# Kernel optimization log

Measured on AMD Instinct MI355X. Metric: run time of the kernel, lower is better.

Reference implementation:

```python
import jax, jax.numpy as jnp
import numpy as np

HID = 512
B, M, N = 32, 2048, 2 * HID  # batch, src_len, 2*hid_size


def setup_inputs() -> dict:
    key = jax.random.key(0)
    ks = jax.random.split(key, 8)
    h_c_hat = jax.random.normal(ks[0], (B, N), dtype=jnp.float32)
    enc_outputs = jax.random.normal(ks[1], (B, M, N), dtype=jnp.float32)
    enc_feature = jax.random.normal(ks[2], (B * M, N), dtype=jnp.float32)
    enc_padding_mask = jnp.zeros((B, M), dtype=jnp.float32)  # 1.0 at PAD positions
    coverage = jax.random.uniform(ks[3], (B, M), dtype=jnp.float32)
    # learned params
    s = 1.0 / np.sqrt(N)
    Wd = jax.random.uniform(ks[4], (N, N), minval=-s, maxval=s, dtype=jnp.float32)  # decode_proj weight
    bd = jax.random.uniform(ks[5], (N,), minval=-s, maxval=s, dtype=jnp.float32)    # decode_proj bias
    wc = jax.random.uniform(ks[6], (N,), minval=-1.0, maxval=1.0, dtype=jnp.float32)  # w_c: Linear(1, 2h) weight
    v = jax.random.uniform(ks[7], (N,), minval=-s, maxval=s, dtype=jnp.float32)       # v: Linear(2h, 1) weight
    return {"h_c_hat": h_c_hat, "enc_outputs": enc_outputs, "enc_feature": enc_feature,
            "enc_padding_mask": enc_padding_mask, "coverage": coverage,
            "Wd": Wd, "bd": bd, "wc": wc, "v": v}


def reference(h_c_hat, enc_outputs, enc_feature, enc_padding_mask, coverage, Wd, bd, wc, v):
    b, m, n = enc_outputs.shape
    dec_feature = h_c_hat @ Wd.T + bd                      # [b, n]
    # enc_feature [b*m, n] + broadcast decoder feature + coverage feature (Linear(1,n) == outer product)
    att = enc_feature.reshape(b, m, n) + dec_feature[:, None, :] + coverage[:, :, None] * wc
    scores = jnp.tanh(att) @ v                             # [b, m]
    attn = jax.nn.softmax(scores, axis=1) * (1.0 - enc_padding_mask)
    attn = attn / attn.sum(axis=1, keepdims=True)          # renormalize after masking
    context_vec = jnp.einsum('bm,bmn->bn', attn, enc_outputs)  # [b, 2h]
    new_coverage = coverage + attn
    return context_vec, attn, new_coverage
```

## Files before the change

### kernel.cpp

```cpp
#include <hip/hip_runtime.h>
#include <math.h>

#define BB 32
#define MM 2048
#define NN 1024
#define C_SCALE 2.88539008177793f
#define L2E 1.44269504088896f

#if __has_builtin(__builtin_amdgcn_exp2f)
#define EXP2F(x) __builtin_amdgcn_exp2f(x)
#else
#define EXP2F(x) exp2f(x)
#endif
#if __has_builtin(__builtin_amdgcn_rcpf)
#define RCPF(x) __builtin_amdgcn_rcpf(x)
#else
#define RCPF(x) (1.0f / (x))
#endif

__device__ __forceinline__ float waveReduceSum(float x) {
#pragma unroll
    for (int off = 32; off > 0; off >>= 1) x += __shfl_xor(x, off, 64);
    return x;
}
__device__ __forceinline__ float waveReduceMax(float x) {
#pragma unroll
    for (int off = 32; off > 0; off >>= 1) x = fmaxf(x, __shfl_xor(x, off, 64));
    return x;
}

__global__ __launch_bounds__(256) void k_dec(const float* __restrict__ h,
                                             const float* __restrict__ Wd,
                                             const float* __restrict__ bd,
                                             float* __restrict__ dec_s) {
    const int n = blockIdx.x;
    const int t = threadIdx.x;
    const int lane = t & 63, wave = t >> 6;
    const float4 wd4 = *(const float4*)(Wd + (size_t)n * NN + t * 4);
    __shared__ float red[BB][4];
#pragma unroll
    for (int b = 0; b < BB; ++b) {
        const float4 h4 = *(const float4*)(h + b * NN + t * 4);
        float p = wd4.x * h4.x + wd4.y * h4.y + wd4.z * h4.z + wd4.w * h4.w;
        p = waveReduceSum(p);
        if (lane == 0) red[b][wave] = p;
    }
    __syncthreads();
    if (t < BB) {
        float s = red[t][0] + red[t][1] + red[t][2] + red[t][3];
        dec_s[t * NN + n] = (s + bd[n]) * C_SCALE;
    }
}

__global__ __launch_bounds__(256) void k_scores(const float* __restrict__ ef,
                                                const float* __restrict__ dec_s,
                                                const float* __restrict__ wc,
                                                const float* __restrict__ v,
                                                const float* __restrict__ cov,
                                                float* __restrict__ scores) {
    const int t = threadIdx.x;
    const int lane = t & 63, wave = t >> 6;
    const int b = blockIdx.x >> 5;
    const int mblk = blockIdx.x & 31;
    const int m0 = mblk * 64 + wave * 16;

    float4 dec4[4], wcs4[4], v4[4];
#pragma unroll
    for (int it = 0; it < 4; ++it) {
        const int k = it * 256 + lane * 4;
        dec4[it] = *(const float4*)(dec_s + b * NN + k);
        float4 w = *(const float4*)(wc + k);
        wcs4[it] = make_float4(w.x * C_SCALE, w.y * C_SCALE, w.z * C_SCALE, w.w * C_SCALE);
        v4[it] = *(const float4*)(v + k);
    }

    for (int mm = 0; mm < 16; ++mm) {
        const int m = m0 + mm;
        const float cv = cov[b * MM + m];
        const float* row = ef + (size_t)(b * MM + m) * NN;
        float acc = 0.f;
#pragma unroll
        for (int it = 0; it < 4; ++it) {
            const float4 e4 = *(const float4*)(row + it * 256 + lane * 4);
            {
                float x = fmaf(C_SCALE, e4.x, dec4[it].x); x = fmaf(cv, wcs4[it].x, x);
                float r = RCPF(EXP2F(x) + 1.0f);
                acc = fmaf(fmaf(-2.0f, r, 1.0f), v4[it].x, acc);
            }
            {
                float x = fmaf(C_SCALE, e4.y, dec4[it].y); x = fmaf(cv, wcs4[it].y, x);
                float r = RCPF(EXP2F(x) + 1.0f);
                acc = fmaf(fmaf(-2.0f, r, 1.0f), v4[it].y, acc);
            }
            {
                float x = fmaf(C_SCALE, e4.z, dec4[it].z); x = fmaf(cv, wcs4[it].z, x);
                float r = RCPF(EXP2F(x) + 1.0f);
                acc = fmaf(fmaf(-2.0f, r, 1.0f), v4[it].z, acc);
            }
            {
                float x = fmaf(C_SCALE, e4.w, dec4[it].w); x = fmaf(cv, wcs4[it].w, x);
                float r = RCPF(EXP2F(x) + 1.0f);
                acc = fmaf(fmaf(-2.0f, r, 1.0f), v4[it].w, acc);
            }
        }
        acc = waveReduceSum(acc);
        if (lane == 0) scores[b * MM + m] = acc;
    }
}

__global__ __launch_bounds__(256) void k_softmax(const float* __restrict__ scores,
                                                 const float* __restrict__ mask,
                                                 const float* __restrict__ cov,
                                                 float* __restrict__ attn_out,
                                                 float* __restrict__ cov_out) {
    const int b = blockIdx.x;
    const int t = threadIdx.x;
    const int lane = t & 63, wave = t >> 6;
    __shared__ float red[4];

    float s[8];
    float mx = -3.0e38f;
#pragma unroll
    for (int i = 0; i < 8; ++i) {
        s[i] = scores[b * MM + i * 256 + t];
        mx = fmaxf(mx, s[i]);
    }
    mx = waveReduceMax(mx);
    if (lane == 0) red[wave] = mx;
    __syncthreads();
    mx = fmaxf(fmaxf(red[0], red[1]), fmaxf(red[2], red[3]));
    __syncthreads();

    float g[8];
    float ls = 0.f;
#pragma unroll
    for (int i = 0; i < 8; ++i) {
        float keep = 1.0f - mask[b * MM + i * 256 + t];
        g[i] = EXP2F((s[i] - mx) * L2E) * keep;
        ls += g[i];
    }
    ls = waveReduceSum(ls);
    if (lane == 0) red[wave] = ls;
    __syncthreads();
    const float S = red[0] + red[1] + red[2] + red[3];
    const float inv = RCPF(S);
#pragma unroll
    for (int i = 0; i < 8; ++i) {
        const int idx = b * MM + i * 256 + t;
        const float a = g[i] * inv;
        attn_out[idx] = a;
        cov_out[idx] = cov[idx] + a;
    }
}

__global__ __launch_bounds__(256) void k_ctx_partial(const float* __restrict__ eo,
                                                     const float* __restrict__ attn,
                                                     float* __restrict__ part) {
    const int b = blockIdx.x >> 6;
    const int p = blockIdx.x & 63;
    const int t = threadIdx.x;
    const int n = t * 4;
    const float* base = eo + ((size_t)b * MM + p * 32) * NN + n;
    float4 acc = make_float4(0.f, 0.f, 0.f, 0.f);
#pragma unroll 4
    for (int mm = 0; mm < 32; ++mm) {
        const float a = attn[b * MM + p * 32 + mm];
        const float4 e = *(const float4*)(base + (size_t)mm * NN);
        acc.x = fmaf(a, e.x, acc.x);
        acc.y = fmaf(a, e.y, acc.y);
        acc.z = fmaf(a, e.z, acc.z);
        acc.w = fmaf(a, e.w, acc.w);
    }
    *(float4*)(part + ((size_t)(b * 64 + p)) * NN + n) = acc;
}

__global__ __launch_bounds__(256) void k_ctx_reduce(const float* __restrict__ part,
                                                    float* __restrict__ ctx) {
    const int idx = blockIdx.x * 256 + threadIdx.x;
    const int b = idx >> 10;
    const int n = idx & 1023;
    float s = 0.f;
#pragma unroll 8
    for (int p = 0; p < 64; ++p) s += part[((size_t)(b * 64 + p)) * NN + n];
    ctx[idx] = s;
}

extern "C" void kernel_launch(void* const* d_in, const int* in_sizes, int n_in,
                              void* d_out, int out_size, void* d_ws, size_t ws_size,
                              hipStream_t stream) {
    const float* h    = (const float*)d_in[0];
    const float* eo   = (const float*)d_in[1];
    const float* ef   = (const float*)d_in[2];
    const float* mask = (const float*)d_in[3];
    const float* cov  = (const float*)d_in[4];
    const float* Wd   = (const float*)d_in[5];
    const float* bd   = (const float*)d_in[6];
    const float* wc   = (const float*)d_in[7];
    const float* v    = (const float*)d_in[8];

    float* out  = (float*)d_out;
    float* ctx  = out;
    float* attn = out + BB * NN;
    float* ncov = attn + BB * MM;

    float* dec_s  = (float*)d_ws;
    float* scores = dec_s + BB * NN;
    float* part   = scores + BB * MM;

    k_dec<<<NN, 256, 0, stream>>>(h, Wd, bd, dec_s);
    k_scores<<<BB * 32, 256, 0, stream>>>(ef, dec_s, wc, v, cov, scores);
    k_softmax<<<BB, 256, 0, stream>>>(scores, mask, cov, attn, ncov);
    k_ctx_partial<<<BB * 64, 256, 0, stream>>>(eo, attn, part);
    k_ctx_reduce<<<(BB * NN) / 256, 256, 0, stream>>>(part, ctx);
}
```

Before: 544.9 us.

## Fuse softmax into score and context kernels using partial exp sums

Removes the standalone softmax kernel. The scores kernel now computes unnormalized exp(score)*keep directly, without subtracting the row max, and writes per-block partial sums. The context kernel reduces those partial sums to a normalizer, scales the weights on the fly, and writes attn and the new coverage. The scores grid is also split into twice as many blocks, each covering half as many rows. This saves a launch and a pass over the scores, but without the max subtraction exp can overflow if scores get large.

```diff
diff --git a/kernel.cpp b/kernel.cpp
--- a/kernel.cpp
+++ b/kernel.cpp
@@ -21,11 +21,6 @@
 __device__ __forceinline__ float waveReduceSum(float x) {
 #pragma unroll
     for (int off = 32; off > 0; off >>= 1) x += __shfl_xor(x, off, 64);
-    return x;
-}
-__device__ __forceinline__ float waveReduceMax(float x) {
-#pragma unroll
-    for (int off = 32; off > 0; off >>= 1) x = fmaxf(x, __shfl_xor(x, off, 64));
     return x;
 }
 
@@ -57,12 +52,14 @@
                                                 const float* __restrict__ wc,
                                                 const float* __restrict__ v,
                                                 const float* __restrict__ cov,
-                                                float* __restrict__ scores) {
+                                                const float* __restrict__ mask,
+                                                float* __restrict__ g,
+                                                float* __restrict__ psum) {
     const int t = threadIdx.x;
     const int lane = t & 63, wave = t >> 6;
-    const int b = blockIdx.x >> 5;
-    const int mblk = blockIdx.x & 31;
-    const int m0 = mblk * 64 + wave * 16;
+    const int b = blockIdx.x >> 6;
+    const int mblk = blockIdx.x & 63;
+    const int m0 = mblk * 32 + wave * 8;
 
     float4 dec4[4], wcs4[4], v4[4];
 #pragma unroll
@@ -74,7 +71,9 @@
         v4[it] = *(const float4*)(v + k);
     }
 
-    for (int mm = 0; mm < 16; ++mm) {
+    __shared__ float wsum[4];
+    float gs = 0.f;
+    for (int mm = 0; mm < 8; ++mm) {
         const int m = m0 + mm;
         const float cv = cov[b * MM + m];
         const float* row = ef + (size_t)(b * MM + m) * NN;
@@ -104,67 +103,49 @@
             }
         }
         acc = waveReduceSum(acc);
-        if (lane == 0) scores[b * MM + m] = acc;
+        if (lane == 0) {
+            const float keep = 1.0f - mask[b * MM + m];
+            const float gg = EXP2F(acc * L2E) * keep;
+            g[b * MM + m] = gg;
+            gs += gg;
+        }
     }
-}
-
-__global__ __launch_bounds__(256) void k_softmax(const float* __restrict__ scores,
-                                                 const float* __restrict__ mask,
-                                                 const float* __restrict__ cov,
-                                                 float* __restrict__ attn_out,
-                                                 float* __restrict__ cov_out) {
-    const int b = blockIdx.x;
-    const int t = threadIdx.x;
-    const int lane = t & 63, wave = t >> 6;
-    __shared__ float red[4];
-
-    float s[8];
-    float mx = -3.0e38f;
-#pragma unroll
-    for (int i = 0; i < 8; ++i) {
-        s[i] = scores[b * MM + i * 256 + t];
-        mx = fmaxf(mx, s[i]);
-    }
-    mx = waveReduceMax(mx);
-    if (lane == 0) red[wave] = mx;
+    if (lane == 0) wsum[wave] = gs;
     __syncthreads();
-    mx = fmaxf(fmaxf(red[0], red[1]), fmaxf(red[2], red[3]));
-    __syncthreads();
-
-    float g[8];
-    float ls = 0.f;
-#pragma unroll
-    for (int i = 0; i < 8; ++i) {
-        float keep = 1.0f - mask[b * MM + i * 256 + t];
-        g[i] = EXP2F((s[i] - mx) * L2E) * keep;
-        ls += g[i];
-    }
-    ls = waveReduceSum(ls);
-    if (lane == 0) red[wave] = ls;
-    __syncthreads();
-    const float S = red[0] + red[1] + red[2] + red[3];
-    const float inv = RCPF(S);
-#pragma unroll
-    for (int i = 0; i < 8; ++i) {
-        const int idx = b * MM + i * 256 + t;
-        const float a = g[i] * inv;
-        attn_out[idx] = a;
-        cov_out[idx] = cov[idx] + a;
-    }
+    if (t == 0) psum[b * 64 + mblk] = wsum[0] + wsum[1] + wsum[2] + wsum[3];
 }
 
 __global__ __launch_bounds__(256) void k_ctx_partial(const float* __restrict__ eo,
-                                                     const float* __restrict__ attn,
+                                                     const float* __restrict__ g,
+                                                     const float* __restrict__ psum,
+                                                     const float* __restrict__ cov,
+                                                     float* __restrict__ attn,
+                                                     float* __restrict__ ncov,
                                                      float* __restrict__ part) {
     const int b = blockIdx.x >> 6;
     const int p = blockIdx.x & 63;
     const int t = threadIdx.x;
+    __shared__ float sInv;
+    if (t < 64) {
+        float x = psum[b * 64 + t];
+        x = waveReduceSum(x);
+        if (t == 0) sInv = 1.0f / x;
+    }
+    __syncthreads();
+    const float inv = sInv;
+    if (t < 32) {
+        const int idx = b * MM + p * 32 + t;
+        const float a = g[idx] * inv;
+        attn[idx] = a;
+        ncov[idx] = cov[idx] + a;
+    }
     const int n = t * 4;
     const float* base = eo + ((size_t)b * MM + p * 32) * NN + n;
+    const float* grow = g + b * MM + p * 32;
     float4 acc = make_float4(0.f, 0.f, 0.f, 0.f);
 #pragma unroll 4
     for (int mm = 0; mm < 32; ++mm) {
-        const float a = attn[b * MM + p * 32 + mm];
+        const float a = grow[mm] * inv;
         const float4 e = *(const float4*)(base + (size_t)mm * NN);
         acc.x = fmaf(a, e.x, acc.x);
         acc.y = fmaf(a, e.y, acc.y);
@@ -203,13 +184,13 @@
     float* attn = out + BB * NN;
     float* ncov = attn + BB * MM;
 
-    float* dec_s  = (float*)d_ws;
-    float* scores = dec_s + BB * NN;
-    float* part   = scores + BB * MM;
+    float* dec_s = (float*)d_ws;
+    float* g     = dec_s + BB * NN;
+    float* psum  = g + BB * MM;
+    float* part  = psum + BB * 64;
 
     k_dec<<<NN, 256, 0, stream>>>(h, Wd, bd, dec_s);
-    k_scores<<<BB * 32, 256, 0, stream>>>(ef, dec_s, wc, v, cov, scores);
-    k_softmax<<<BB, 256, 0, stream>>>(scores, mask, cov, attn, ncov);
-    k_ctx_partial<<<BB * 64, 256, 0, stream>>>(eo, attn, part);
+    k_scores<<<BB * 64, 256, 0, stream>>>(ef, dec_s, wc, v, cov, mask, g, psum);
+    k_ctx_partial<<<BB * 64, 256, 0, stream>>>(eo, g, psum, cov, attn, ncov, part);
     k_ctx_reduce<<<(BB * NN) / 256, 256, 0, stream>>>(part, ctx);
 }
```

Result: no change. 546.7 us (+0.3%).
